# Kernel tuning notes

Hardware: AMD Instinct MI355X
Metric: run time of the kernel (lower is better)

Reference implementation:

```python
import jax, jax.numpy as jnp
import numpy as np

# config (matches init_kwargs)
B, L, Q = 4, 2048, 2048      # batch, memory_length, query_len
H, D = 16, 64                # heads, head_dim
E = H * D                    # hidden_dim = 1024
NB = 512                     # num_basis
SIGMAS = np.array([0.005, 0.01])
RIDGE = 0.5
CLAMP_MIN = 1e-4


def _build_basis():
    # torch.meshgrid(linspace(0,1,NB//2), sigmas) then flatten: mu repeated, sigma tiled
    mu = np.repeat(np.linspace(0.0, 1.0, NB // len(SIGMAS)), len(SIGMAS))
    sg = np.tile(SIGMAS, NB // len(SIGMAS))
    return mu, sg


def _build_G(mu, sg):
    # get_positions(L, padding=True), L even: 2L points in [-0.5+shift, 1.5-shift]
    shift = 1.0 / (2 * L)
    pos = np.linspace(-0.5 + shift, 1.5 - shift, 2 * L)
    # F[j, p] = N(pos_p; mu_j, sg_j)
    Fm = np.exp(-0.5 * ((pos[None, :] - mu[:, None]) / sg[:, None]) ** 2) / (sg[:, None] * np.sqrt(2 * np.pi))
    G = Fm.T @ np.linalg.inv(Fm @ Fm.T + RIDGE * np.eye(NB))  # [2L, NB]
    return G[L // 2:-(L // 2)]  # [L, NB]


def setup_inputs() -> dict:
    key = jax.random.key(0)
    ks = jax.random.split(key, 8)
    mu, sg = _build_basis()
    G = _build_G(mu, sg)
    s_e = 1.0 / np.sqrt(E)
    s_n = 1.0 / np.sqrt(NB)
    return {
        "k": jax.random.normal(ks[0], (B, L, E), jnp.float32),
        "q": jax.random.normal(ks[1], (B, Q, E), jnp.float32),
        "Wq": jax.random.normal(ks[2], (E, E), jnp.float32) * s_e,
        "Wk": jax.random.normal(ks[3], (E, E), jnp.float32) * s_e,
        "Wv": jax.random.normal(ks[4], (E, E), jnp.float32) * s_e,
        "Wo": jax.random.normal(ks[5], (E, E), jnp.float32) * s_e,
        "w_mu": jax.random.normal(ks[6], (NB,), jnp.float32) * s_n,
        "w_sigma": jax.random.normal(ks[7], (NB,), jnp.float32) * s_n,
        "Gs": jnp.asarray(G, jnp.float32),
        "basis_mu": jnp.asarray(mu, jnp.float32),
        "basis_sigma": jnp.asarray(sg, jnp.float32),
    }


def reference(k, q, Wq, Wk, Wv, Wo, w_mu, w_sigma, Gs, basis_mu, basis_sigma):
    # continuous compression of the memory: B_mat[b,n,e] = sum_l k[b,l,e] * Gs[l,n]
    Bm = jnp.einsum('ble,ln->bne', k, Gs)  # [B, NB, E]
    keys = (Bm @ Wk.T).reshape(B, NB, H, D).transpose(0, 2, 1, 3)   # [B,H,NB,D]
    vals = (Bm @ Wv.T).reshape(B, NB, H, D).transpose(0, 2, 1, 3)   # [B,H,NB,D]
    qry = (q @ Wq.T).reshape(B, Q, H, D).transpose(0, 2, 1, 3)      # [B,H,Q,D]
    # scores over basis functions
    scores = jnp.einsum('bhqd,bhnd->bhqn', qry, keys) / jnp.sqrt(jnp.float32(D))
    # affine heads -> Gaussian attention density parameters per query
    mu_q = jax.nn.sigmoid(scores @ w_mu)[..., None]                         # [B,H,Q,1]
    sig2 = jnp.clip(jax.nn.softplus(scores @ w_sigma), CLAMP_MIN)[..., None]  # [B,H,Q,1]
    # continuous softmax closed form: r_j = N(mu_q; basis_mu_j, sig2 + basis_sigma_j^2)
    var = sig2 + basis_sigma ** 2                                           # [B,H,Q,NB]
    r = jnp.exp(-0.5 * (mu_q - basis_mu) ** 2 / var) / jnp.sqrt(2.0 * jnp.pi * var)
    ctx = jnp.einsum('bhqn,bhnd->bhqd', r, vals)                            # [B,H,Q,D]
    ctx = ctx.transpose(0, 2, 1, 3).reshape(B, Q, E)
    return ctx @ Wo.T
```

## Files before the change

### kernel.cpp

```cpp
#include <hip/hip_runtime.h>

#define BB 4
#define LL 2048
#define QQ 2048
#define HH 16
#define DD 64
#define EE 1024
#define NB 512

typedef __attribute__((ext_vector_type(8))) short bf16x8;
typedef __attribute__((ext_vector_type(4))) float f32x4;

__device__ inline ushort bf16_rne(float f) {
  __bf16 b = static_cast<__bf16>(f);
  return __builtin_bit_cast(ushort, b);
}
__device__ inline float bf16_f(ushort h) { return __uint_as_float((uint)h << 16); }
__device__ inline void hilo(float x, ushort& h, ushort& l) {
  h = bf16_rne(x);
  l = bf16_rne(x - bf16_f(h));
}

__device__ inline void cvt8_pack(const float* a, uint4& ph, uint4& pl) {
  ushort h[8], l[8];
  #pragma unroll
  for (int j = 0; j < 8; j++) hilo(a[j], h[j], l[j]);
  ph = make_uint4((uint)h[0] | ((uint)h[1] << 16), (uint)h[2] | ((uint)h[3] << 16),
                  (uint)h[4] | ((uint)h[5] << 16), (uint)h[6] | ((uint)h[7] << 16));
  pl = make_uint4((uint)l[0] | ((uint)l[1] << 16), (uint)l[2] | ((uint)l[3] << 16),
                  (uint)l[4] | ((uint)l[5] << 16), (uint)l[6] | ((uint)l[7] << 16));
}

__device__ inline void xcd_remap(int& bx, int& by, int& bz) {
  int gx = gridDim.x, gy = gridDim.y;
  int nwg = gx * gy * (int)gridDim.z;
  int lin = blockIdx.x + gx * (blockIdx.y + gy * blockIdx.z);
  int swz = (lin & 7) * (nwg >> 3) + (lin >> 3);
  bx = swz % gx; int tmp = swz / gx; by = tmp % gy; bz = tmp / gy;
}

__global__ __launch_bounds__(256) void cvt_hilo(
    const float* __restrict__ x, ushort* __restrict__ hi, ushort* __restrict__ lo, long n)
{
  long i0 = ((long)blockIdx.x * 256 + threadIdx.x) * 8;
  long stride = (long)gridDim.x * 2048;
  for (long i = i0; i < n; i += stride) {
    float a[8];
    *(float4*)&a[0] = *(const float4*)&x[i];
    *(float4*)&a[4] = *(const float4*)&x[i + 4];
    uint4 ph, pl;
    cvt8_pack(a, ph, pl);
    *(uint4*)&hi[i] = ph;
    *(uint4*)&lo[i] = pl;
  }
}

__global__ __launch_bounds__(256) void cvt_hiloT(
    const float* __restrict__ x, ushort* __restrict__ hiT, ushort* __restrict__ loT,
    int R, int C, long zIn, long zOut)
{
  x += (long)blockIdx.z * zIn; hiT += (long)blockIdx.z * zOut; loT += (long)blockIdx.z * zOut;
  __shared__ float tile[32][33];
  const int t = threadIdx.x;
  const long r0 = (long)blockIdx.y * 32, c0 = (long)blockIdx.x * 32;
  {
    int row = t >> 3, c4 = t & 7;
    float4 v = *(const float4*)&x[(r0 + row) * C + c0 + c4 * 4];
    tile[row][c4*4+0] = v.x; tile[row][c4*4+1] = v.y;
    tile[row][c4*4+2] = v.z; tile[row][c4*4+3] = v.w;
  }
  __syncthreads();
  {
    int col = t >> 3, r4 = t & 7;
    ushort h[4], l[4];
    #pragma unroll
    for (int j = 0; j < 4; j++) hilo(tile[r4 * 4 + j][col], h[j], l[j]);
    uint2 ph = make_uint2((uint)h[0] | ((uint)h[1] << 16), (uint)h[2] | ((uint)h[3] << 16));
    uint2 pl = make_uint2((uint)l[0] | ((uint)l[1] << 16), (uint)l[2] | ((uint)l[3] << 16));
    long o = (c0 + col) * (long)R + r0 + r4 * 4;
    *(uint2*)&hiT[o] = ph;
    *(uint2*)&loT[o] = pl;
  }
}

__global__ __launch_bounds__(256) void add_pairs(
    float* __restrict__ dst, long dstStride,
    const float* __restrict__ src, long srcPairStride, long n)
{
  float* d = dst + (long)blockIdx.z * dstStride;
  const float* s0 = src + (long)blockIdx.z * srcPairStride;
  const float* s1 = s0 + n;
  long i0 = ((long)blockIdx.x * 256 + threadIdx.x) * 4;
  long stride = (long)gridDim.x * 1024;
  for (long i = i0; i < n; i += stride) {
    float4 a = *(const float4*)&s0[i];
    float4 b = *(const float4*)&s1[i];
    a.x += b.x; a.y += b.y; a.z += b.z; a.w += b.w;
    *(float4*)&d[i] = a;
  }
}


__global__ __launch_bounds__(256) void gemm_nt128(
    const float* __restrict__ A, const float* __restrict__ B, float* __restrict__ C,
    int N, int K, long sA, long sB, long sC, int NS, int Kc)
{
  const int z = blockIdx.z;
  const int b = z / NS, ks = z - b * NS;
  A += (long)b * sA + (long)ks * Kc;
  B += (long)b * sB + (long)ks * Kc;
  C += (long)z * sC;
  __shared__ float As[32][132], Bs[32][132];
  const int t = threadIdx.x;
  const int tx = t & 15, ty = t >> 4;
  const long m0 = (long)blockIdx.y * 128, n0 = (long)blockIdx.x * 128;
  float acc[8][8] = {};
  for (int k0 = 0; k0 < Kc; k0 += 32) {
    #pragma unroll
    for (int i = 0; i < 4; i++) {
      int f = t + i * 256;
      int r = f >> 3, k4 = f & 7;
      float4 va = *(const float4*)&A[(m0 + r) * K + k0 + k4 * 4];
      As[k4*4+0][r] = va.x; As[k4*4+1][r] = va.y; As[k4*4+2][r] = va.z; As[k4*4+3][r] = va.w;
      float4 vb = *(const float4*)&B[(n0 + r) * K + k0 + k4 * 4];
      Bs[k4*4+0][r] = vb.x; Bs[k4*4+1][r] = vb.y; Bs[k4*4+2][r] = vb.z; Bs[k4*4+3][r] = vb.w;
    }
    __syncthreads();
    #pragma unroll
    for (int kk = 0; kk < 32; kk++) {
      float4 a0 = *(const float4*)&As[kk][ty*8];
      float4 a1 = *(const float4*)&As[kk][ty*8+4];
      float4 b0 = *(const float4*)&Bs[kk][tx*8];
      float4 b1 = *(const float4*)&Bs[kk][tx*8+4];
      float ar[8] = {a0.x,a0.y,a0.z,a0.w,a1.x,a1.y,a1.z,a1.w};
      float br[8] = {b0.x,b0.y,b0.z,b0.w,b1.x,b1.y,b1.z,b1.w};
      #pragma unroll
      for (int i = 0; i < 8; i++)
        #pragma unroll
        for (int j = 0; j < 8; j++)
          acc[i][j] += ar[i] * br[j];
    }
    __syncthreads();
  }
  #pragma unroll
  for (int i = 0; i < 8; i++) {
    float4 o0 = make_float4(acc[i][0], acc[i][1], acc[i][2], acc[i][3]);
    float4 o1 = make_float4(acc[i][4], acc[i][5], acc[i][6], acc[i][7]);
    *(float4*)&C[(m0 + ty*8 + i) * N + n0 + tx*8    ] = o0;
    *(float4*)&C[(m0 + ty*8 + i) * N + n0 + tx*8 + 4] = o1;
  }
}

__global__ __launch_bounds__(256) void gemm_tn128(
    const float* __restrict__ A, const float* __restrict__ B, float* __restrict__ C,
    int M, int N, long sA, long sB, long sC, int NS, int Kc)
{
  const int z = blockIdx.z;
  const int b = z / NS, ks = z - b * NS;
  A += (long)b * sA + (long)ks * Kc * M;
  B += (long)b * sB + (long)ks * Kc * N;
  C += (long)z * sC;
  __shared__ float As[32][132], Bs[32][132];
  const int t = threadIdx.x;
  const int tx = t & 15, ty = t >> 4;
  const long m0 = (long)blockIdx.y * 128, n0 = (long)blockIdx.x * 128;
  float acc[8][8] = {};
  for (int k0 = 0; k0 < Kc; k0 += 32) {
    #pragma unroll
    for (int i = 0; i < 4; i++) {
      int f = t + i * 256;
      int r = f >> 5, c4 = f & 31;
      *(float4*)&As[r][c4 * 4] = *(const float4*)&A[(long)(k0 + r) * M + m0 + c4 * 4];
      *(float4*)&Bs[r][c4 * 4] = *(const float4*)&B[(long)(k0 + r) * N + n0 + c4 * 4];
    }
    __syncthreads();
    #pragma unroll
    for (int kk = 0; kk < 32; kk++) {
      float4 a0 = *(const float4*)&As[kk][ty*8];
      float4 a1 = *(const float4*)&As[kk][ty*8+4];
      float4 b0 = *(const float4*)&Bs[kk][tx*8];
      float4 b1 = *(const float4*)&Bs[kk][tx*8+4];
      float ar[8] = {a0.x,a0.y,a0.z,a0.w,a1.x,a1.y,a1.z,a1.w};
      float br[8] = {b0.x,b0.y,b0.z,b0.w,b1.x,b1.y,b1.z,b1.w};
      #pragma unroll
      for (int i = 0; i < 8; i++)
        #pragma unroll
        for (int j = 0; j < 8; j++)
          acc[i][j] += ar[i] * br[j];
    }
    __syncthreads();
  }
  #pragma unroll
  for (int i = 0; i < 8; i++) {
    float4 o0 = make_float4(acc[i][0], acc[i][1], acc[i][2], acc[i][3]);
    float4 o1 = make_float4(acc[i][4], acc[i][5], acc[i][6], acc[i][7]);
    *(float4*)&C[(m0 + ty*8 + i) * N + n0 + tx*8    ] = o0;
    *(float4*)&C[(m0 + ty*8 + i) * N + n0 + tx*8 + 4] = o1;
  }
}

__global__ __launch_bounds__(256) void gemm_nt64(
    const float* __restrict__ A, const float* __restrict__ B, float* __restrict__ C,
    int M, int N, int K, long sA, long sB, long sC)
{
  A += (long)blockIdx.z * sA; B += (long)blockIdx.z * sB; C += (long)blockIdx.z * sC;
  __shared__ float As[32][68], Bs[32][68];
  const int t = threadIdx.x;
  const int tx = t & 15, ty = t >> 4;
  const int m0 = blockIdx.y * 64, n0 = blockIdx.x * 64;
  float acc[4][4] = {};
  for (int k0 = 0; k0 < K; k0 += 32) {
    #pragma unroll
    for (int i = 0; i < 2; i++) {
      int f = t + i * 256;
      int r = f >> 3, k4 = f & 7;
      float4 va = *(const float4*)&A[(long)(m0 + r) * K + k0 + k4 * 4];
      As[k4*4+0][r] = va.x; As[k4*4+1][r] = va.y; As[k4*4+2][r] = va.z; As[k4*4+3][r] = va.w;
      float4 vb = *(const float4*)&B[(long)(n0 + r) * K + k0 + k4 * 4];
      Bs[k4*4+0][r] = vb.x; Bs[k4*4+1][r] = vb.y; Bs[k4*4+2][r] = vb.z; Bs[k4*4+3][r] = vb.w;
    }
    __syncthreads();
    #pragma unroll
    for (int kk = 0; kk < 32; kk++) {
      float4 a4 = *(const float4*)&As[kk][ty * 4];
      float4 b4 = *(const float4*)&Bs[kk][tx * 4];
      float ar[4] = {a4.x, a4.y, a4.z, a4.w};
      float br[4] = {b4.x, b4.y, b4.z, b4.w};
      #pragma unroll
      for (int i = 0; i < 4; i++)
        #pragma unroll
        for (int j = 0; j < 4; j++)
          acc[i][j] += ar[i] * br[j];
    }
    __syncthreads();
  }
  #pragma unroll
  for (int i = 0; i < 4; i++) {
    float4 o = make_float4(acc[i][0], acc[i][1], acc[i][2], acc[i][3]);
    *(float4*)&C[(long)(m0 + ty*4 + i) * N + n0 + tx*4] = o;
  }
}


__global__ __launch_bounds__(256) void gemm_nt128_b3(
    const ushort* __restrict__ Ah, const ushort* __restrict__ Al,
    const ushort* __restrict__ Bh, const ushort* __restrict__ Bl,
    float* __restrict__ C, int N, int K, long sA, long sC, int NS, int Kc)
{
  int bx, by, bz;
  xcd_remap(bx, by, bz);
  const int zb = bz / NS, ks = bz - zb * NS;
  Ah += (long)zb * sA + (long)ks * Kc;
  Al += (long)zb * sA + (long)ks * Kc;
  Bh += (long)ks * Kc;
  Bl += (long)ks * Kc;
  C  += (long)bz * sC;
  __shared__ ushort AhS[2][4096], AlS[2][4096], BhS[2][4096], BlS[2][4096];
  const int t = threadIdx.x;
  const int l = t & 63, w = t >> 6;
  const long m0 = (long)by * 128, n0 = (long)bx * 128;
  const int frA = (w & 1) * 4;
  const int frB = (w >> 1) * 4;
  const int rs = ((((l & 15) ^ ((l >> 4) << 1)) + 16 * (l >> 4))) * 8;
  const int row0 = t >> 2, kq0 = t & 3;
  const long gA0 = (m0 + row0) * (long)K + kq0 * 8, gA1 = gA0 + 64 * (long)K;
  const long gB0 = (n0 + row0) * (long)K + kq0 * 8, gB1 = gB0 + 64 * (long)K;
  const int d0 = (row0 >> 4) * 512 + ((((row0 & 15) ^ (kq0 << 1)) + 16 * kq0)) * 8;
  const int d1 = d0 + 2048;
  uint4 rA0h, rA1h, rA0l, rA1l, rB0h, rB1h, rB0l, rB1l;
  rA0h = *(const uint4*)(Ah + gA0); rA1h = *(const uint4*)(Ah + gA1);
  rA0l = *(const uint4*)(Al + gA0); rA1l = *(const uint4*)(Al + gA1);
  rB0h = *(const uint4*)(Bh + gB0); rB1h = *(const uint4*)(Bh + gB1);
  rB0l = *(const uint4*)(Bl + gB0); rB1l = *(const uint4*)(Bl + gB1);
  *(uint4*)&AhS[0][d0] = rA0h; *(uint4*)&AhS[0][d1] = rA1h;
  *(uint4*)&AlS[0][d0] = rA0l; *(uint4*)&AlS[0][d1] = rA1l;
  *(uint4*)&BhS[0][d0] = rB0h; *(uint4*)&BhS[0][d1] = rB1h;
  *(uint4*)&BlS[0][d0] = rB0l; *(uint4*)&BlS[0][d1] = rB1l;
  __syncthreads();
  f32x4 acc[4][4] = {};
  int cur = 0;
  for (int k0 = 32; k0 < Kc; k0 += 32) {
    rA0h = *(const uint4*)(Ah + gA0 + k0); rA1h = *(const uint4*)(Ah + gA1 + k0);
    rA0l = *(const uint4*)(Al + gA0 + k0); rA1l = *(const uint4*)(Al + gA1 + k0);
    rB0h = *(const uint4*)(Bh + gB0 + k0); rB1h = *(const uint4*)(Bh + gB1 + k0);
    rB0l = *(const uint4*)(Bl + gB0 + k0); rB1l = *(const uint4*)(Bl + gB1 + k0);
    {
      const ushort* ahp = AhS[cur]; const ushort* alp = AlS[cur];
      const ushort* bhp = BhS[cur]; const ushort* blp = BlS[cur];
      bf16x8 ah[4], al[4], bh[4], bl[4];
      #pragma unroll
      for (int i = 0; i < 4; i++) {
        ah[i] = *(const bf16x8*)&ahp[(frA + i) * 512 + rs];
        al[i] = *(const bf16x8*)&alp[(frA + i) * 512 + rs];
        bh[i] = *(const bf16x8*)&bhp[(frB + i) * 512 + rs];
        bl[i] = *(const bf16x8*)&blp[(frB + i) * 512 + rs];
      }
      #pragma unroll
      for (int i = 0; i < 4; i++)
        #pragma unroll
        for (int j = 0; j < 4; j++) {
          acc[i][j] = __builtin_amdgcn_mfma_f32_16x16x32_bf16(ah[i], bh[j], acc[i][j], 0, 0, 0);
          acc[i][j] = __builtin_amdgcn_mfma_f32_16x16x32_bf16(ah[i], bl[j], acc[i][j], 0, 0, 0);
          acc[i][j] = __builtin_amdgcn_mfma_f32_16x16x32_bf16(al[i], bh[j], acc[i][j], 0, 0, 0);
        }
    }
    const int nxt = cur ^ 1;
    *(uint4*)&AhS[nxt][d0] = rA0h; *(uint4*)&AhS[nxt][d1] = rA1h;
    *(uint4*)&AlS[nxt][d0] = rA0l; *(uint4*)&AlS[nxt][d1] = rA1l;
    *(uint4*)&BhS[nxt][d0] = rB0h; *(uint4*)&BhS[nxt][d1] = rB1h;
    *(uint4*)&BlS[nxt][d0] = rB0l; *(uint4*)&BlS[nxt][d1] = rB1l;
    __syncthreads();
    cur = nxt;
  }
  {
    const ushort* ahp = AhS[cur]; const ushort* alp = AlS[cur];
    const ushort* bhp = BhS[cur]; const ushort* blp = BlS[cur];
    bf16x8 ah[4], al[4], bh[4], bl[4];
    #pragma unroll
    for (int i = 0; i < 4; i++) {
      ah[i] = *(const bf16x8*)&ahp[(frA + i) * 512 + rs];
      al[i] = *(const bf16x8*)&alp[(frA + i) * 512 + rs];
      bh[i] = *(const bf16x8*)&bhp[(frB + i) * 512 + rs];
      bl[i] = *(const bf16x8*)&blp[(frB + i) * 512 + rs];
    }
    #pragma unroll
    for (int i = 0; i < 4; i++)
      #pragma unroll
      for (int j = 0; j < 4; j++) {
        acc[i][j] = __builtin_amdgcn_mfma_f32_16x16x32_bf16(ah[i], bh[j], acc[i][j], 0, 0, 0);
        acc[i][j] = __builtin_amdgcn_mfma_f32_16x16x32_bf16(ah[i], bl[j], acc[i][j], 0, 0, 0);
        acc[i][j] = __builtin_amdgcn_mfma_f32_16x16x32_bf16(al[i], bh[j], acc[i][j], 0, 0, 0);
      }
  }
  const long rbase = m0 + (w & 1) * 64 + (l >> 4) * 4;
  const int  cbase = (int)n0 + (w >> 1) * 64 + (l & 15);
  #pragma unroll
  for (int i = 0; i < 4; i++)
    #pragma unroll
    for (int j = 0; j < 4; j++)
      #pragma unroll
      for (int r = 0; r < 4; r++)
        C[(rbase + i * 16 + r) * N + cbase + j * 16] = acc[i][j][r];
}

__global__ __launch_bounds__(256) void gemm_nt64x64_b3_us(
    const ushort* __restrict__ Ah, const ushort* __restrict__ Al,
    const ushort* __restrict__ Bh, const ushort* __restrict__ Bl,
    ushort* __restrict__ Ch, ushort* __restrict__ Cl, int N, int K, long sB, long sC)
{
  int bx, by, bz;
  xcd_remap(bx, by, bz);
  Bh += (long)bz * sB; Bl += (long)bz * sB;
  Ch += (long)bz * sC; Cl += (long)bz * sC;
  __shared__ ushort AhS[2][2048], AlS[2][2048], BhS[2][2048], BlS[2][2048];
  const int t = threadIdx.x;
  const int l = t & 63, w = t >> 6;
  const long m0 = (long)by * 64, n0 = (long)bx * 64;
  const int wm = w & 1, wn = w >> 1;
  const int rs = ((((l & 15) ^ ((l >> 4) << 1)) + 16 * (l >> 4))) * 8;
  const int row0 = t >> 2, kq0 = t & 3;
  const long gA0 = (m0 + row0) * (long)K + kq0 * 8;
  const long gB0 = (n0 + row0) * (long)K + kq0 * 8;
  const int d0 = (row0 >> 4) * 512 + ((((row0 & 15) ^ (kq0 << 1)) + 16 * kq0)) * 8;
  uint4 rAh, rAl, rBh, rBl;
  rAh = *(const uint4*)(Ah + gA0);
  rAl = *(const uint4*)(Al + gA0);
  rBh = *(const uint4*)(Bh + gB0);
  rBl = *(const uint4*)(Bl + gB0);
  *(uint4*)&AhS[0][d0] = rAh; *(uint4*)&AlS[0][d0] = rAl;
  *(uint4*)&BhS[0][d0] = rBh; *(uint4*)&BlS[0][d0] = rBl;
  __syncthreads();
  f32x4 acc[2][2] = {};
  int cur = 0;
  for (int k0 = 32; k0 < K; k0 += 32) {
    rAh = *(const uint4*)(Ah + gA0 + k0);
    rAl = *(const uint4*)(Al + gA0 + k0);
    rBh = *(const uint4*)(Bh + gB0 + k0);
    rBl = *(const uint4*)(Bl + gB0 + k0);
    {
      const ushort* ahp = AhS[cur]; const ushort* alp = AlS[cur];
      const ushort* bhp = BhS[cur]; const ushort* blp = BlS[cur];
      bf16x8 ah[2], al[2], bh[2], bl[2];
      #pragma unroll
      for (int i = 0; i < 2; i++) {
        ah[i] = *(const bf16x8*)&ahp[(wm * 2 + i) * 512 + rs];
        al[i] = *(const bf16x8*)&alp[(wm * 2 + i) * 512 + rs];
        bh[i] = *(const bf16x8*)&bhp[(wn * 2 + i) * 512 + rs];
        bl[i] = *(const bf16x8*)&blp[(wn * 2 + i) * 512 + rs];
      }
      #pragma unroll
      for (int i = 0; i < 2; i++)
        #pragma unroll
        for (int j = 0; j < 2; j++) {
          acc[i][j] = __builtin_amdgcn_mfma_f32_16x16x32_bf16(ah[i], bh[j], acc[i][j], 0, 0, 0);
          acc[i][j] = __builtin_amdgcn_mfma_f32_16x16x32_bf16(ah[i], bl[j], acc[i][j], 0, 0, 0);
          acc[i][j] = __builtin_amdgcn_mfma_f32_16x16x32_bf16(al[i], bh[j], acc[i][j], 0, 0, 0);
        }
    }
    const int nxt = cur ^ 1;
    *(uint4*)&AhS[nxt][d0] = rAh; *(uint4*)&AlS[nxt][d0] = rAl;
    *(uint4*)&BhS[nxt][d0] = rBh; *(uint4*)&BlS[nxt][d0] = rBl;
    __syncthreads();
    cur = nxt;
  }
  {
    const ushort* ahp = AhS[cur]; const ushort* alp = AlS[cur];
    const ushort* bhp = BhS[cur]; const ushort* blp = BlS[cur];
    bf16x8 ah[2], al[2], bh[2], bl[2];
    #pragma unroll
    for (int i = 0; i < 2; i++) {
      ah[i] = *(const bf16x8*)&ahp[(wm * 2 + i) * 512 + rs];
      al[i] = *(const bf16x8*)&alp[(wm * 2 + i) * 512 + rs];
      bh[i] = *(const bf16x8*)&bhp[(wn * 2 + i) * 512 + rs];
      bl[i] = *(const bf16x8*)&blp[(wn * 2 + i) * 512 + rs];
    }
    #pragma unroll
    for (int i = 0; i < 2; i++)
      #pragma unroll
      for (int j = 0; j < 2; j++) {
        acc[i][j] = __builtin_amdgcn_mfma_f32_16x16x32_bf16(ah[i], bh[j], acc[i][j], 0, 0, 0);
        acc[i][j] = __builtin_amdgcn_mfma_f32_16x16x32_bf16(ah[i], bl[j], acc[i][j], 0, 0, 0);
        acc[i][j] = __builtin_amdgcn_mfma_f32_16x16x32_bf16(al[i], bh[j], acc[i][j], 0, 0, 0);
      }
  }
  const long rbase = m0 + wm * 32 + (l >> 4) * 4;
  const int  cbase = (int)n0 + wn * 32 + (l & 15);
  #pragma unroll
  for (int i = 0; i < 2; i++)
    #pragma unroll
    for (int j = 0; j < 2; j++)
      #pragma unroll
      for (int r = 0; r < 4; r++) {
        long off = (rbase + i * 16 + r) * N + cbase + j * 16;
        ushort hb, lb;
        hilo(acc[i][j][r], hb, lb);
        Ch[off] = hb;
        Cl[off] = lb;
      }
}

__global__ __launch_bounds__(256) void nb_ctx_mf(
    const ushort* __restrict__ vTh, const ushort* __restrict__ vTl,
    const float* __restrict__ muq, const float* __restrict__ sg2,
    const float* __restrict__ bmu, const float* __restrict__ bsg,
    ushort* __restrict__ ctxh, ushort* __restrict__ ctxl,
    long sMu, long sC, long sV)
{
  int bx, by, bz;
  xcd_remap(bx, by, bz);
  const int h = by, b = bz;
  const long q0 = (long)bx * 128;
  const int t = threadIdx.x;
  const int l = t & 63, w = t >> 6, wm = w & 1, wn = w >> 1;
  __shared__ ushort AhS[4096], AlS[4096];
  __shared__ ushort BhS[2048], BlS[2048];
  __shared__ float mu_s[128], s2_s[128], bm_s[NB];
  const float* muqb = muq + (long)b * sMu;
  const float* sg2b = sg2 + (long)b * sMu;
  if (t < 128) {
    mu_s[t] = muqb[(long)h * QQ + q0 + t];
    s2_s[t] = sg2b[(long)h * QQ + q0 + t];
  }
  for (int i = t; i < NB; i += 256) bm_s[i] = bmu[i];
  const float b0 = bsg[0], b1 = bsg[1];
  const float bv0 = b0 * b0, bv1 = b1 * b1;
  __syncthreads();
  const ushort* vThb = vTh + (long)b * sV + (long)(h * 64) * NB;
  const ushort* vTlb = vTl + (long)b * sV + (long)(h * 64) * NB;
  const int rs = ((((l & 15) ^ ((l >> 4) << 1)) + 16 * (l >> 4))) * 8;
  const int srow = t >> 2, skq = t & 3;
  const long bsrc = (long)srow * NB + skq * 8;
  const int bdst = (srow >> 4) * 512 + ((((srow & 15) ^ (skq << 1)) + 16 * skq)) * 8;
  float m_[2], si0_[2], si1_[2], c0_[2], c1_[2];
  #pragma unroll
  for (int p = 0; p < 2; p++) {
    int s = t + p * 256;
    int lf = s & 63;
    int qq = ((s >> 6) << 4) + (lf & 15);
    float s2 = s2_s[qq];
    m_[p] = mu_s[qq];
    si0_[p] = __builtin_amdgcn_rsqf(s2 + bv0);
    si1_[p] = __builtin_amdgcn_rsqf(s2 + bv1);
    c0_[p] = si0_[p] * 0.3989422804014327f;
    c1_[p] = si1_[p] * 0.3989422804014327f;
  }
  f32x4 acc[4][2] = {};
  for (int c = 0; c < 16; c++) {
    *(uint4*)&BhS[bdst] = *(const uint4*)(vThb + bsrc + c * 32);
    *(uint4*)&BlS[bdst] = *(const uint4*)(vTlb + bsrc + c * 32);
    #pragma unroll
    for (int p = 0; p < 2; p++) {
      int s = t + p * 256;
      int lf = s & 63;
      int nb0 = c * 32 + (lf >> 4) * 8;
      float a[8];
      #pragma unroll
      for (int e = 0; e < 8; e++) {
        float d = m_[p] - bm_s[nb0 + e];
        float si = (e & 1) ? si1_[p] : si0_[p];
        float cc = (e & 1) ? c1_[p] : c0_[p];
        float tt = d * si;
        a[e] = __expf(tt * tt * -0.5f) * cc;
      }
      uint4 ph, pl;
      cvt8_pack(a, ph, pl);
      *(uint4*)&AhS[s * 8] = ph;
      *(uint4*)&AlS[s * 8] = pl;
    }
    __syncthreads();
    bf16x8 bhf[2], blf[2];
    #pragma unroll
    for (int j = 0; j < 2; j++) {
      bhf[j] = *(const bf16x8*)&BhS[(wn * 2 + j) * 512 + rs];
      blf[j] = *(const bf16x8*)&BlS[(wn * 2 + j) * 512 + rs];
    }
    #pragma unroll
    for (int i = 0; i < 4; i++) {
      bf16x8 ah = *(const bf16x8*)&AhS[(wm * 4 + i) * 512 + l * 8];
      bf16x8 al = *(const bf16x8*)&AlS[(wm * 4 + i) * 512 + l * 8];
      #pragma unroll
      for (int j = 0; j < 2; j++) {
        acc[i][j] = __builtin_amdgcn_mfma_f32_16x16x32_bf16(ah, bhf[j], acc[i][j], 0, 0, 0);
        acc[i][j] = __builtin_amdgcn_mfma_f32_16x16x32_bf16(ah, blf[j], acc[i][j], 0, 0, 0);
        acc[i][j] = __builtin_amdgcn_mfma_f32_16x16x32_bf16(al, bhf[j], acc[i][j], 0, 0, 0);
      }
    }
    __syncthreads();
  }
  ushort* ch = ctxh + (long)b * sC;
  ushort* cl = ctxl + (long)b * sC;
  const long rbase = q0 + wm * 64 + (l >> 4) * 4;
  const int  cbase = h * 64 + wn * 32 + (l & 15);
  #pragma unroll
  for (int i = 0; i < 4; i++)
    #pragma unroll
    for (int j = 0; j < 2; j++)
      #pragma unroll
      for (int r = 0; r < 4; r++) {
        long off = (rbase + i * 16 + r) * EE + cbase + j * 16;
        ushort hb, lb;
        hilo(acc[i][j][r], hb, lb);
        ch[off] = hb;
        cl[off] = lb;
      }
}

__global__ __launch_bounds__(256) void nb_uvec_us(
    const ushort* __restrict__ Bmh, const ushort* __restrict__ Bml,
    const float* __restrict__ wmu, const float* __restrict__ wsg,
    float* __restrict__ ump, float* __restrict__ usp, long sBm, long sU)
{
  Bmh += (long)blockIdx.z * sBm; Bml += (long)blockIdx.z * sBm;
  ump += (long)blockIdx.z * sU; usp += (long)blockIdx.z * sU;
  const int e = blockIdx.x * 256 + threadIdx.x;
  const int c = blockIdx.y;
  float am = 0.f, as = 0.f;
  #pragma unroll 8
  for (int n = c * 64; n < c * 64 + 64; n++) {
    float bv = bf16_f(Bmh[(long)n * EE + e]) + bf16_f(Bml[(long)n * EE + e]);
    am += wmu[n] * bv;
    as += wsg[n] * bv;
  }
  ump[(long)c * EE + e] = am;
  usp[(long)c * EE + e] = as;
}

__global__ __launch_bounds__(256) void nb_uvec(
    const float* __restrict__ Bm, const float* __restrict__ wmu, const float* __restrict__ wsg,
    float* __restrict__ ump, float* __restrict__ usp, long sBm, long sU)
{
  Bm += (long)blockIdx.z * sBm; ump += (long)blockIdx.z * sU; usp += (long)blockIdx.z * sU;
  const int e = blockIdx.x * 256 + threadIdx.x;
  const int c = blockIdx.y;
  float am = 0.f, as = 0.f;
  #pragma unroll 8
  for (int n = c * 64; n < c * 64 + 64; n++) {
    float bv = Bm[(long)n * EE + e];
    am += wmu[n] * bv;
    as += wsg[n] * bv;
  }
  ump[(long)c * EE + e] = am;
  usp[(long)c * EE + e] = as;
}

__global__ __launch_bounds__(256) void nb_kw(
    const float* __restrict__ Wk, const float* __restrict__ ump, const float* __restrict__ usp,
    float* __restrict__ kwm, float* __restrict__ kws, long sU, long sK)
{
  ump += (long)blockIdx.z * sU; usp += (long)blockIdx.z * sU;
  kwm += (long)blockIdx.z * sK; kws += (long)blockIdx.z * sK;
  __shared__ float pm[256], ps[256];
  const int e = blockIdx.x, t = threadIdx.x;
  const float* row = Wk + (long)e * EE;
  float am = 0.f, as = 0.f;
  for (int i = t; i < EE; i += 256) {
    float um = 0.f, us = 0.f;
    #pragma unroll
    for (int c = 0; c < 8; c++) { um += ump[(long)c * EE + i]; us += usp[(long)c * EE + i]; }
    float w = row[i];
    am += w * um;
    as += w * us;
  }
  pm[t] = am; ps[t] = as;
  __syncthreads();
  for (int s = 128; s > 0; s >>= 1) {
    if (t < s) { pm[t] += pm[t + s]; ps[t] += ps[t + s]; }
    __syncthreads();
  }
  if (t == 0) { kwm[e] = pm[0]; kws[e] = ps[0]; }
}

__global__ __launch_bounds__(256) void nb_amas(
    const float* __restrict__ Wq, const float* __restrict__ kwm, const float* __restrict__ kws,
    float* __restrict__ AmAs, long sK, long sAm)
{
  kwm += (long)blockIdx.z * sK; kws += (long)blockIdx.z * sK;
  AmAs += (long)blockIdx.z * sAm;
  __shared__ float km[64], ks[64];
  const int t = threadIdx.x;
  const int h = blockIdx.y;
  const int e = blockIdx.x * 256 + t;
  if (t < 64) { km[t] = kwm[h * 64 + t]; ks[t] = kws[h * 64 + t]; }
  __syncthreads();
  float am = 0.f, as = 0.f;
  #pragma unroll 8
  for (int d = 0; d < 64; d++) {
    float w = Wq[(long)(h * 64 + d) * EE + e];
    am += km[d] * w;
    as += ks[d] * w;
  }
  AmAs[(long)e * 32 + h]      = am;
  AmAs[(long)e * 32 + 16 + h] = as;
}

__global__ __launch_bounds__(256) void nb_musig8(
    const float* __restrict__ qb, const float* __restrict__ AmAs,
    float* __restrict__ muq, float* __restrict__ sg2, long sQ, long sAm, long sMu)
{
  qb += (long)blockIdx.z * sQ; AmAs += (long)blockIdx.z * sAm;
  muq += (long)blockIdx.z * sMu; sg2 += (long)blockIdx.z * sMu;
  __shared__ float qs[8 * EE];
  const int t = threadIdx.x;
  const long q0 = (long)blockIdx.x * 8;
  for (int i = t * 4; i < 8 * EE; i += 1024)
    *(float4*)&qs[i] = *(const float4*)&qb[q0 * EE + i];
  __syncthreads();
  const int o = t & 31, row = t >> 5;
  const float* qr = qs + row * EE;
  float acc = 0.f;
  #pragma unroll 8
  for (int e = 0; e < EE; e++)
    acc += qr[e] * AmAs[(long)e * 32 + o];
  float s = acc * 0.125f;
  if (o < 16) {
    muq[(long)o * QQ + q0 + row] = 1.f / (1.f + expf(-s));
  } else {
    float sp = (s > 20.f) ? s : log1pf(expf(s));
    sg2[(long)(o - 16) * QQ + q0 + row] = fmaxf(sp, 1e-4f);
  }
}

__global__ __launch_bounds__(256) void nb_musig(
    const float* __restrict__ qb, const float* __restrict__ AmAs,
    float* __restrict__ muq, float* __restrict__ sg2, long sQ, long sAm, long sMu)
{
  qb += (long)blockIdx.z * sQ; AmAs += (long)blockIdx.z * sAm;
  muq += (long)blockIdx.z * sMu; sg2 += (long)blockIdx.z * sMu;
  __shared__ float qs[EE];
  __shared__ float part[8][32];
  const int t = threadIdx.x, qrow = blockIdx.x;
  for (int i = t; i < EE; i += 256) qs[i] = qb[(long)qrow * EE + i];
  __syncthreads();
  const int o = t & 31, ch = t >> 5;
  float acc = 0.f;
  const int e0 = ch * 128;
  #pragma unroll 8
  for (int i = 0; i < 128; i++) {
    int e = e0 + i;
    acc += qs[e] * AmAs[(long)e * 32 + o];
  }
  part[ch][o] = acc;
  __syncthreads();
  if (t < 32) {
    float s = 0.f;
    #pragma unroll
    for (int c = 0; c < 8; c++) s += part[c][o];
    s *= 0.125f;
    if (o < 16) {
      muq[(long)o * QQ + qrow] = 1.f / (1.f + expf(-s));
    } else {
      float sp = (s > 20.f) ? s : log1pf(expf(s));
      sg2[(long)(o - 16) * QQ + qrow] = fmaxf(sp, 1e-4f);
    }
  }
}

__global__ __launch_bounds__(128) void nb_ctx128(
    const float* __restrict__ vals, const float* __restrict__ muq, const float* __restrict__ sg2,
    const float* __restrict__ bmu,  const float* __restrict__ bsg, float* __restrict__ ctx,
    long sV, long sMu, long sC)
{
  vals += (long)blockIdx.z * sV; ctx += (long)blockIdx.z * sC;
  muq += (long)blockIdx.z * sMu; sg2 += (long)blockIdx.z * sMu;
  __shared__ float As[32][132], Bs[32][68];
  __shared__ __align__(16) float mu_s[128], s2_s[128];
  const int t = threadIdx.x;
  const int tx = t & 7, ty = t >> 3;
  const long q0 = (long)blockIdx.x * 128;
  const int h = blockIdx.y;
  mu_s[t] = muq[(long)h * QQ + q0 + t];
  s2_s[t] = sg2[(long)h * QQ + q0 + t];
  __syncthreads();
  float acc[8][8] = {};
  for (int n0 = 0; n0 < NB; n0 += 32) {
    #pragma unroll
    for (int i = 0; i < 4; i++) {
      int f = t + i * 128;
      int r = f >> 4, c4 = f & 15;
      *(float4*)&Bs[r][c4 * 4] = *(const float4*)&vals[(long)(n0 + r) * EE + h * 64 + c4 * 4];
    }
    #pragma unroll
    for (int i = 0; i < 8; i++) {
      int idx = t + i * 128;
      int n = idx >> 5, qg = idx & 31;
      float bm = bmu[n0 + n], bs = bsg[n0 + n];
      float bs2 = bs * bs;
      float4 m4 = *(const float4*)&mu_s[qg * 4];
      float4 s4 = *(const float4*)&s2_s[qg * 4];
      float4 rr;
      {
        float v0 = s4.x + bs2, d0 = m4.x - bm;
        float v1 = s4.y + bs2, d1 = m4.y - bm;
        float v2 = s4.z + bs2, d2 = m4.z - bm;
        float v3 = s4.w + bs2, d3 = m4.w - bm;
        float r0 = __builtin_amdgcn_rcpf(v0), r1 = __builtin_amdgcn_rcpf(v1);
        float r2 = __builtin_amdgcn_rcpf(v2), r3 = __builtin_amdgcn_rcpf(v3);
        rr.x = __expf(d0 * d0 * r0 * -0.5f) * __builtin_amdgcn_rsqf(v0 * 6.2831853071795865f);
        rr.y = __expf(d1 * d1 * r1 * -0.5f) * __builtin_amdgcn_rsqf(v1 * 6.2831853071795865f);
        rr.z = __expf(d2 * d2 * r2 * -0.5f) * __builtin_amdgcn_rsqf(v2 * 6.2831853071795865f);
        rr.w = __expf(d3 * d3 * r3 * -0.5f) * __builtin_amdgcn_rsqf(v3 * 6.2831853071795865f);
      }
      *(float4*)&As[n][qg * 4] = rr;
    }
    __syncthreads();
    #pragma unroll
    for (int kk = 0; kk < 32; kk++) {
      float4 a0 = *(const float4*)&As[kk][ty*8];
      float4 a1 = *(const float4*)&As[kk][ty*8+4];
      float4 b0 = *(const float4*)&Bs[kk][tx*8];
      float4 b1 = *(const float4*)&Bs[kk][tx*8+4];
      float ar[8] = {a0.x,a0.y,a0.z,a0.w,a1.x,a1.y,a1.z,a1.w};
      float br[8] = {b0.x,b0.y,b0.z,b0.w,b1.x,b1.y,b1.z,b1.w};
      #pragma unroll
      for (int i = 0; i < 8; i++)
        #pragma unroll
        for (int j = 0; j < 8; j++)
          acc[i][j] += ar[i] * br[j];
    }
    __syncthreads();
  }
  #pragma unroll
  for (int i = 0; i < 8; i++) {
    float4 o0 = make_float4(acc[i][0], acc[i][1], acc[i][2], acc[i][3]);
    float4 o1 = make_float4(acc[i][4], acc[i][5], acc[i][6], acc[i][7]);
    *(float4*)&ctx[(q0 + ty*8 + i) * EE + h * 64 + tx*8    ] = o0;
    *(float4*)&ctx[(q0 + ty*8 + i) * EE + h * 64 + tx*8 + 4] = o1;
  }
}

extern "C" void kernel_launch(void* const* d_in, const int* in_sizes, int n_in,
                              void* d_out, int out_size, void* d_ws, size_t ws_size,
                              hipStream_t stream) {
  const float* k   = (const float*)d_in[0];
  const float* q   = (const float*)d_in[1];
  const float* Wq  = (const float*)d_in[2];
  const float* Wk  = (const float*)d_in[3];
  const float* Wv  = (const float*)d_in[4];
  const float* Wo  = (const float*)d_in[5];
  const float* wmu = (const float*)d_in[6];
  const float* wsg = (const float*)d_in[7];
  const float* Gs  = (const float*)d_in[8];
  const float* bmu = (const float*)d_in[9];
  const float* bsg = (const float*)d_in[10];
  float* out = (float*)d_out;
  char* ws = (char*)d_ws;

  const long sBm = (long)NB * EE;
  const long sU  = 8L * EE;
  const long sK  = EE;
  const long sAm = 32L * EE;
  const long sMu = (long)HH * QQ;
  const long sQ  = (long)QQ * EE;

  if (ws_size >= (50u << 20)) {
    ushort* kTh  = (ushort*)(ws + 0);
    ushort* kTl  = (ushort*)(ws + (16u << 20));
    ushort* GsTh = (ushort*)(ws + (32u << 20));
    ushort* GsTl = (ushort*)(ws + (34u << 20));
    ushort* Bmh  = (ushort*)(ws + (40u << 20));
    ushort* Bml  = (ushort*)(ws + (44u << 20));
    ushort* Wvh  = (ushort*)(ws + 0);
    ushort* Wvl  = (ushort*)(ws + (2u << 20));
    ushort* vTh  = (ushort*)(ws + (32u << 20));
    ushort* vTl  = (ushort*)(ws + (36u << 20));
    ushort* Woh  = (ushort*)(ws + (32u << 20));
    ushort* Wol  = (ushort*)(ws + (34u << 20));
    ushort* ctxh = (ushort*)(ws + 0);
    ushort* ctxl = (ushort*)(ws + (16u << 20));
    char*  sm    = ws + (48u << 20);
    float* ump4  = (float*)(sm);
    float* usp4  = (float*)(sm + (128u << 10));
    float* kwm4  = (float*)(sm + (256u << 10));
    float* kws4  = (float*)(sm + (272u << 10));
    float* AmAs4 = (float*)(sm + (288u << 10));
    float* muq4  = (float*)(sm + (800u << 10));
    float* sg24  = (float*)(sm + (1312u << 10));

    cvt_hiloT<<<dim3(NB/32, LL/32, 1),  256, 0, stream>>>(Gs, GsTh, GsTl, LL, NB, 0L, 0L);
    cvt_hiloT<<<dim3(EE/32, LL/32, BB), 256, 0, stream>>>(k, kTh, kTl, LL, EE,
                                                          (long)LL*EE, (long)LL*EE);
    gemm_nt64x64_b3_us<<<dim3(EE/64, NB/64, BB), 256, 0, stream>>>(
        GsTh, GsTl, kTh, kTl, Bmh, Bml, EE, LL, (long)LL*EE, sBm);
    nb_uvec_us<<<dim3(EE/256, 8, BB),  256, 0, stream>>>(Bmh, Bml, wmu, wsg, ump4, usp4, sBm, sU);
    nb_kw     <<<dim3(EE, 1, BB),      256, 0, stream>>>(Wk, ump4, usp4, kwm4, kws4, sU, sK);
    nb_amas   <<<dim3(EE/256, HH, BB), 256, 0, stream>>>(Wq, kwm4, kws4, AmAs4, sK, sAm);
    nb_musig8 <<<dim3(QQ/8, 1, BB),    256, 0, stream>>>(q, AmAs4, muq4, sg24, sQ, sAm, sMu);
    cvt_hilo<<<dim3(256), 256, 0, stream>>>(Wv, Wvh, Wvl, (long)EE * EE);
    gemm_nt64x64_b3_us<<<dim3(NB/64, EE/64, BB), 256, 0, stream>>>(
        Wvh, Wvl, Bmh, Bml, vTh, vTl, NB, EE, sBm, sBm);
    nb_ctx_mf<<<dim3(QQ/128, HH, BB), 256, 0, stream>>>(
        vTh, vTl, muq4, sg24, bmu, bsg, ctxh, ctxl, sMu, sQ, sBm);
    cvt_hilo<<<dim3(256), 256, 0, stream>>>(Wo, Woh, Wol, (long)EE * EE);
    gemm_nt128_b3<<<dim3(EE/128, QQ/128, BB), 256, 0, stream>>>(
        ctxh, ctxl, Woh, Wol, out, EE, EE, sQ, sQ, 1, EE);
  } else {
    float* BmP   = (float*)(ws + 0);
    float* ctxS  = (float*)(ws + 0);
    float* vals4 = (float*)(ws + (16u << 20));
    char*  sm    = ws + (24u << 20);
    float* ump4  = (float*)(sm);
    float* usp4  = (float*)(sm + (128u << 10));
    float* kwm4  = (float*)(sm + (256u << 10));
    float* kws4  = (float*)(sm + (272u << 10));
    float* AmAs4 = (float*)(sm + (288u << 10));
    float* muq4  = (float*)(sm + (800u << 10));
    float* sg24  = (float*)(sm + (1312u << 10));

    gemm_tn128<<<dim3(EE/128, NB/128, BB*2), 256, 0, stream>>>(
        Gs, k, BmP, NB, EE, 0L, (long)LL*EE, sBm, 2, LL/2);
    add_pairs<<<dim3(256, 1, BB), 256, 0, stream>>>(BmP, 2*sBm, BmP, 2*sBm, sBm);
    gemm_nt128<<<dim3(EE/128, NB/128, BB), 256, 0, stream>>>(
        BmP, Wv, vals4, EE, EE, 2*sBm, 0L, sBm, 1, EE);
    nb_uvec  <<<dim3(EE/256, 8, BB),  256, 0, stream>>>(BmP, wmu, wsg, ump4, usp4, 2*sBm, sU);
    nb_kw    <<<dim3(EE, 1, BB),      256, 0, stream>>>(Wk, ump4, usp4, kwm4, kws4, sU, sK);
    nb_amas  <<<dim3(EE/256, HH, BB), 256, 0, stream>>>(Wq, kwm4, kws4, AmAs4, sK, sAm);
    nb_musig <<<dim3(QQ, 1, BB),      256, 0, stream>>>(q, AmAs4, muq4, sg24, sQ, sAm, sMu);
    for (int b = 0; b < BB; b++) {
      nb_ctx128<<<dim3(QQ/128, HH, 1), 128, 0, stream>>>(
          vals4 + (long)b*sBm, muq4 + (long)b*sMu, sg24 + (long)b*sMu,
          bmu, bsg, ctxS, 0L, 0L, 0L);
      gemm_nt64<<<dim3(EE/64, QQ/64, 1), 256, 0, stream>>>(
          ctxS, Wo, out + (long)b*sQ, QQ, EE, EE, 0L, 0L, 0L);
    }
  }
  (void)in_sizes; (void)n_in; (void)out_size;
}
```

Measured before the change: 360.4 us.

## Double-buffer LDS in nb_ctx_mf to overlap A generation with MFMA

The context kernel now keeps two LDS buffers for the generated Gaussian weights and the V tiles. The next chunk's V global loads and exp-based weight generation are issued into registers while MFMAs run on the current buffer, and one barrier per iteration replaces two. This is meant to hide global load latency and transcendental ALU work behind matrix ops, at the cost of double the LDS footprint and more live registers, which could lower occupancy.

New measurement: 364.0 us. No clear change (+1.0%).

```diff
diff --git a/kernel.cpp b/kernel.cpp
--- a/kernel.cpp
+++ b/kernel.cpp
@@ -452,8 +452,8 @@
   const long q0 = (long)bx * 128;
   const int t = threadIdx.x;
   const int l = t & 63, w = t >> 6, wm = w & 1, wn = w >> 1;
-  __shared__ ushort AhS[4096], AlS[4096];
-  __shared__ ushort BhS[2048], BlS[2048];
+  __shared__ ushort AhS[2][4096], AlS[2][4096];
+  __shared__ ushort BhS[2][2048], BlS[2][2048];
   __shared__ float mu_s[128], s2_s[128], bm_s[NB];
   const float* muqb = muq + (long)b * sMu;
   const float* sg2b = sg2 + (long)b * sMu;
@@ -484,10 +484,8 @@
     c0_[p] = si0_[p] * 0.3989422804014327f;
     c1_[p] = si1_[p] * 0.3989422804014327f;
   }
-  f32x4 acc[4][2] = {};
-  for (int c = 0; c < 16; c++) {
-    *(uint4*)&BhS[bdst] = *(const uint4*)(vThb + bsrc + c * 32);
-    *(uint4*)&BlS[bdst] = *(const uint4*)(vTlb + bsrc + c * 32);
+  uint4 aPh0, aPl0, aPh1, aPl1, rBh, rBl;
+  auto genA = [&](int c) {
     #pragma unroll
     for (int p = 0; p < 2; p++) {
       int s = t + p * 256;
@@ -504,20 +502,63 @@
       }
       uint4 ph, pl;
       cvt8_pack(a, ph, pl);
-      *(uint4*)&AhS[s * 8] = ph;
-      *(uint4*)&AlS[s * 8] = pl;
-    }
-    __syncthreads();
+      if (p == 0) { aPh0 = ph; aPl0 = pl; } else { aPh1 = ph; aPl1 = pl; }
+    }
+  };
+  rBh = *(const uint4*)(vThb + bsrc);
+  rBl = *(const uint4*)(vTlb + bsrc);
+  genA(0);
+  *(uint4*)&AhS[0][t * 8] = aPh0;        *(uint4*)&AhS[0][(t + 256) * 8] = aPh1;
+  *(uint4*)&AlS[0][t * 8] = aPl0;        *(uint4*)&AlS[0][(t + 256) * 8] = aPl1;
+  *(uint4*)&BhS[0][bdst] = rBh;          *(uint4*)&BlS[0][bdst] = rBl;
+  __syncthreads();
+  f32x4 acc[4][2] = {};
+  int cur = 0;
+  for (int c = 0; c < 15; c++) {
+    rBh = *(const uint4*)(vThb + bsrc + (c + 1) * 32);
+    rBl = *(const uint4*)(vTlb + bsrc + (c + 1) * 32);
+    genA(c + 1);
+    {
+      const ushort* ahp = AhS[cur]; const ushort* alp = AlS[cur];
+      const ushort* bhp = BhS[cur]; const ushort* blp = BlS[cur];
+      bf16x8 bhf[2], blf[2];
+      #pragma unroll
+      for (int j = 0; j < 2; j++) {
+        bhf[j] = *(const bf16x8*)&bhp[(wn * 2 + j) * 512 + rs];
+        blf[j] = *(const bf16x8*)&blp[(wn * 2 + j) * 512 + rs];
+      }
+      #pragma unroll
+      for (int i = 0; i < 4; i++) {
+        bf16x8 ah = *(const bf16x8*)&ahp[(wm * 4 + i) * 512 + l * 8];
+        bf16x8 al = *(const bf16x8*)&alp[(wm * 4 + i) * 512 + l * 8];
+        #pragma unroll
+        for (int j = 0; j < 2; j++) {
+          acc[i][j] = __builtin_amdgcn_mfma_f32_16x16x32_bf16(ah, bhf[j], acc[i][j], 0, 0, 0);
+          acc[i][j] = __builtin_amdgcn_mfma_f32_16x16x32_bf16(ah, blf[j], acc[i][j], 0, 0, 0);
+          acc[i][j] = __builtin_amdgcn_mfma_f32_16x16x32_bf16(al, bhf[j], acc[i][j], 0, 0, 0);
+        }
+      }
+    }
+    const int nxt = cur ^ 1;
+    *(uint4*)&AhS[nxt][t * 8] = aPh0;      *(uint4*)&AhS[nxt][(t + 256) * 8] = aPh1;
+    *(uint4*)&AlS[nxt][t * 8] = aPl0;      *(uint4*)&AlS[nxt][(t + 256) * 8] = aPl1;
+    *(uint4*)&BhS[nxt][bdst] = rBh;        *(uint4*)&BlS[nxt][bdst] = rBl;
+    __syncthreads();
+    cur = nxt;
+  }
+  {
+    const ushort* ahp = AhS[cur]; const ushort* alp = AlS[cur];
+    const ushort* bhp = BhS[cur]; const ushort* blp = BlS[cur];
     bf16x8 bhf[2], blf[2];
     #pragma unroll
     for (int j = 0; j < 2; j++) {
-      bhf[j] = *(const bf16x8*)&BhS[(wn * 2 + j) * 512 + rs];
-      blf[j] = *(const bf16x8*)&BlS[(wn * 2 + j) * 512 + rs];
+      bhf[j] = *(const bf16x8*)&bhp[(wn * 2 + j) * 512 + rs];
+      blf[j] = *(const bf16x8*)&blp[(wn * 2 + j) * 512 + rs];
     }
     #pragma unroll
     for (int i = 0; i < 4; i++) {
-      bf16x8 ah = *(const bf16x8*)&AhS[(wm * 4 + i) * 512 + l * 8];
-      bf16x8 al = *(const bf16x8*)&AlS[(wm * 4 + i) * 512 + l * 8];
+      bf16x8 ah = *(const bf16x8*)&ahp[(wm * 4 + i) * 512 + l * 8];
+      bf16x8 al = *(const bf16x8*)&alp[(wm * 4 + i) * 512 + l * 8];
       #pragma unroll
       for (int j = 0; j < 2; j++) {
         acc[i][j] = __builtin_amdgcn_mfma_f32_16x16x32_bf16(ah, bhf[j], acc[i][j], 0, 0, 0);
@@ -525,7 +566,6 @@
         acc[i][j] = __builtin_amdgcn_mfma_f32_16x16x32_bf16(al, bhf[j], acc[i][j], 0, 0, 0);
       }
     }
-    __syncthreads();
   }
   ushort* ch = ctxh + (long)b * sC;
   ushort* cl = ctxl + (long)b * sC;
```
